# Optimization experiments

Hardware: AMD Instinct MI355X
Metric: run time of the kernel (lower is better)

Reference implementation:

```python
import jax, jax.numpy as jnp
import numpy as np

N_ATOMS = 50000
N_RES = 6250
C_IN = 30
E_DIM = 12
E_BOND = 150000
E_RAD = 800000
E_RES_RAD = 400000
E_CORR = 20000


def _layer_norm(h, g, b, eps=1e-5):
    mu = h.mean(-1, keepdims=True)
    var = ((h - mu) ** 2).mean(-1, keepdims=True)
    return (h - mu) / jnp.sqrt(var + eps) * g + b


def _mlp(h, W, b, g, beta):
    # Seq(Linear, ReLU, LayerNorm, Dropout) in eval mode (dropout = identity)
    return _layer_norm(jax.nn.relu(h @ W + b), g, beta)


def _point_conv(x, pos, src, dst, W, b, g, beta, num_nodes):
    # PyG PointNetConv with add_self_loops=True, aggr='add'
    loops = jnp.arange(num_nodes)
    s = jnp.concatenate([src, loops])
    d = jnp.concatenate([dst, loops])
    msg = jnp.concatenate([x[s], pos[s] - pos[d]], axis=-1)  # [E+N, F+3]
    h = _mlp(msg, W, b, g, beta)
    return jax.ops.segment_sum(h, d, num_segments=num_nodes)


def _gcne_conv(x, edge_index, edge_attr, W, bias):
    # GCNEConv: gcn_norm with self loops, message = cat(x_j, e) @ W * norm + bias, scatter-add
    n = x.shape[0]
    loops = jnp.arange(n)
    s = jnp.concatenate([edge_index[0], loops])
    d = jnp.concatenate([edge_index[1], loops])
    w_full = jnp.ones(s.shape[0], x.dtype)
    deg = jax.ops.segment_sum(w_full, d, num_segments=n)
    dinv = jnp.where(deg > 0, deg ** -0.5, 0.0)
    norm = dinv[s] * dinv[d]
    ea = jnp.concatenate([edge_attr, jnp.zeros((n, edge_attr.shape[1]), edge_attr.dtype)], axis=0)
    msg = (jnp.concatenate([x[s], ea], axis=-1) @ W) * norm[:, None] + bias
    return jax.ops.segment_sum(msg, d, num_segments=n)


def setup_inputs():
    key = jax.random.key(0)
    ks = jax.random.split(key, 20)
    inp = {}
    inp['x'] = jax.random.normal(ks[0], (N_ATOMS, C_IN), jnp.float32)
    inp['pos'] = jax.random.uniform(ks[1], (N_ATOMS, 3), jnp.float32)
    inp['edge_attr'] = jax.random.normal(ks[2], (E_BOND, E_DIM), jnp.float32)
    inp['edge_index'] = jax.random.randint(ks[3], (2, E_BOND), 0, N_ATOMS)
    inp['rad_edge_index'] = jax.random.randint(ks[4], (2, E_RAD), 0, N_ATOMS)
    inp['res_rad_edge_index'] = jax.random.randint(ks[5], (2, E_RES_RAD), 0, N_RES)
    inp['residue_index'] = jnp.sort(jax.random.randint(ks[6], (N_ATOMS,), 0, N_RES))
    inp['src_idx'] = jax.random.randint(ks[7], (E_CORR,), 0, N_RES)
    inp['tgt_idx'] = jax.random.randint(ks[8], (E_CORR,), 0, N_RES)
    inp['y_lab'] = jax.random.randint(ks[9], (E_CORR,), 0, 2).astype(jnp.int32)
    def glorot(k, shape):
        s = (2.0 / (shape[0] + shape[1])) ** 0.5
        return jax.random.normal(k, shape, jnp.float32) * s
    # conv1 local MLP [3+C_IN -> 64]
    inp['w_pc1'] = glorot(ks[10], (C_IN + 3, 64)); inp['b_pc1'] = jnp.zeros(64)
    inp['g_pc1'] = jnp.ones(64); inp['be_pc1'] = jnp.zeros(64)
    # gcn1 weight [C_IN+E_DIM -> 64]
    inp['w_gcn'] = glorot(ks[11], (C_IN + E_DIM, 64)); inp['b_gcn'] = jnp.zeros(64)
    # atom_embed MLP [64 -> 64]
    inp['w_ae'] = glorot(ks[12], (64, 64)); inp['b_ae'] = jnp.zeros(64)
    inp['g_ae'] = jnp.ones(64); inp['be_ae'] = jnp.zeros(64)
    # res_embed MLP [64 -> 64]
    inp['w_re'] = glorot(ks[13], (64, 64)); inp['b_re'] = jnp.zeros(64)
    inp['g_re'] = jnp.ones(64); inp['be_re'] = jnp.zeros(64)
    # res_conv1 local MLP [3+64 -> 128]
    inp['w_rc'] = glorot(ks[14], (64 + 3, 128)); inp['b_rc'] = jnp.zeros(128)
    inp['g_rc'] = jnp.ones(128); inp['be_rc'] = jnp.zeros(128)
    # res_conv1 global MLP [128 -> 128]
    inp['w_rg'] = glorot(ks[15], (128, 128)); inp['b_rg'] = jnp.zeros(128)
    inp['g_rg'] = jnp.ones(128); inp['be_rg'] = jnp.zeros(128)
    return inp


def reference(x, pos, edge_attr,
              w_pc1, b_pc1, g_pc1, be_pc1,
              w_gcn, b_gcn,
              w_ae, b_ae, g_ae, be_ae,
              w_re, b_re, g_re, be_re,
              w_rc, b_rc, g_rc, be_rc,
              w_rg, b_rg, g_rg, be_rg,
              edge_index, rad_edge_index, res_rad_edge_index,
              residue_index, src_idx, tgt_idx, y_lab):
    n = x.shape[0]
    # SAModule 1: PointConv over atom radius graph, aggr='add', no global_nn
    x1 = _point_conv(x, pos, rad_edge_index[0], rad_edge_index[1],
                     w_pc1, b_pc1, g_pc1, be_pc1, n)
    # GCNEConv over bond graph
    x2 = _gcne_conv(x, edge_index, edge_attr, w_gcn, b_gcn)
    atom_x = _mlp(x1 + x2, w_ae, b_ae, g_ae, be_ae)
    # atom -> residue pooling (global_add_pool / global_mean_pool)
    res_x = jax.ops.segment_sum(atom_x, residue_index, num_segments=N_RES)
    cnt = jax.ops.segment_sum(jnp.ones(n, x.dtype), residue_index, num_segments=N_RES)
    res_pos = jax.ops.segment_sum(pos, residue_index, num_segments=N_RES) / jnp.maximum(cnt, 1.0)[:, None]
    res_x = _mlp(res_x, w_re, b_re, g_re, be_re)
    # SAModule 2: PointConv over residue radius graph with global MLP
    x3 = _point_conv(res_x, res_pos, res_rad_edge_index[0], res_rad_edge_index[1],
                     w_rc, b_rc, g_rc, be_rc, N_RES)
    x3 = _mlp(x3, w_rg, b_rg, g_rg, be_rg)
    # correspondence pairs + CosineEmbeddingLoss(reduction='none')
    x_s = x3[src_idx]
    x_t = x3[tgt_idx]
    y = (2 * y_lab - 1).astype(x.dtype)  # {0,1} -> {-1,+1}
    eps = 1e-8
    cos = (x_s * x_t).sum(-1) / (jnp.maximum(jnp.linalg.norm(x_s, axis=-1), eps) *
                                 jnp.maximum(jnp.linalg.norm(x_t, axis=-1), eps))
    unweighted = jnp.where(y == 1, 1.0 - cos, jnp.maximum(cos, 0.0))
    pos_l = jnp.where(y != 1, 0.0, y)
    neg_l = 1.0 - pos_l
    pos_w = neg_l.sum() / pos_l.sum()
    loss = jnp.mean((pos_l * pos_w + neg_l) * unweighted)
    return loss
```

## Files before the change

kernel.cpp:

```cpp
#include <hip/hip_runtime.h>
#include <math.h>

#define N_ATOMS 50000
#define N_RES 6250
#define C_IN 30
#define E_DIM 12
#define E_BOND 150000
#define E_RAD 800000
#define E_RES_RAD 400000
#define E_CORR 20000

__device__ __forceinline__ int rfl(int v) { return __builtin_amdgcn_readfirstlane(v); }

__device__ __forceinline__ float wsum(float v) {
#pragma unroll
  for (int m = 1; m < 64; m <<= 1) v += __shfl_xor(v, m, 64);
  return v;
}

template <int K>
__global__ void rowmat64(const float* __restrict__ X, const float* __restrict__ W,
                         float* __restrict__ out, int nrows) {
  const int lane = threadIdx.x & 63;
  const int wid = (blockIdx.x * blockDim.x + threadIdx.x) >> 6;
  const int nw = (gridDim.x * blockDim.x) >> 6;
  float wcol[K];
#pragma unroll
  for (int k = 0; k < K; k++) wcol[k] = W[k * 64 + lane];
  for (int r = wid; r < nrows; r += nw) {
    float acc = 0.0f;
#pragma unroll
    for (int k = 0; k < K; k++) acc += X[(size_t)r * K + k] * wcol[k];
    out[(size_t)r * 64 + lane] = acc;
  }
}

__global__ void pc1_edge(const float* __restrict__ xw1, const float* __restrict__ pos,
                         const int* __restrict__ src, const int* __restrict__ dst,
                         const float* __restrict__ W, const float* __restrict__ b,
                         const float* __restrict__ g, const float* __restrict__ be,
                         float* __restrict__ acc) {
  const int lane = threadIdx.x & 63;
  const int wid = (blockIdx.x * blockDim.x + threadIdx.x) >> 6;
  const int nw = (gridDim.x * blockDim.x) >> 6;
  const float w0 = W[(C_IN + 0) * 64 + lane];
  const float w1 = W[(C_IN + 1) * 64 + lane];
  const float w2 = W[(C_IN + 2) * 64 + lane];
  const float bb = b[lane], gg = g[lane], eb = be[lane];
  const int total = E_RAD + N_ATOMS;
  for (int e0 = wid * 2; e0 < total; e0 += nw * 2) {
    const int e1 = e0 + 1;
    int sA, dA, sB, dB;
    float dA0 = 0.0f, dA1 = 0.0f, dA2 = 0.0f, dB0 = 0.0f, dB1 = 0.0f, dB2 = 0.0f;
    if (e0 < E_RAD) {
      sA = rfl(src[e0]); dA = rfl(dst[e0]);
      dA0 = pos[sA * 3 + 0] - pos[dA * 3 + 0];
      dA1 = pos[sA * 3 + 1] - pos[dA * 3 + 1];
      dA2 = pos[sA * 3 + 2] - pos[dA * 3 + 2];
    } else {
      sA = dA = e0 - E_RAD;
    }
    if (e1 < E_RAD) {
      sB = rfl(src[e1]); dB = rfl(dst[e1]);
      dB0 = pos[sB * 3 + 0] - pos[dB * 3 + 0];
      dB1 = pos[sB * 3 + 1] - pos[dB * 3 + 1];
      dB2 = pos[sB * 3 + 2] - pos[dB * 3 + 2];
    } else {
      sB = dB = e1 - E_RAD;
    }
    float hA = xw1[(size_t)sA * 64 + lane] + bb + dA0 * w0 + dA1 * w1 + dA2 * w2;
    float hB = xw1[(size_t)sB * 64 + lane] + bb + dB0 * w0 + dB1 * w1 + dB2 * w2;
    hA = fmaxf(hA, 0.0f);
    hB = fmaxf(hB, 0.0f);
    float s1A = hA, s2A = hA * hA, s1B = hB, s2B = hB * hB;
#pragma unroll
    for (int m = 1; m < 64; m <<= 1) {
      s1A += __shfl_xor(s1A, m, 64);
      s2A += __shfl_xor(s2A, m, 64);
      s1B += __shfl_xor(s1B, m, 64);
      s2B += __shfl_xor(s2B, m, 64);
    }
    const float muA = s1A * (1.0f / 64.0f);
    const float muB = s1B * (1.0f / 64.0f);
    const float vaA = s2A * (1.0f / 64.0f) - muA * muA;
    const float vaB = s2B * (1.0f / 64.0f) - muB * muB;
    const float rA = rsqrtf(vaA + 1e-5f);
    const float rB = rsqrtf(vaB + 1e-5f);
    atomicAdd(&acc[(size_t)dA * 64 + lane], (hA - muA) * rA * gg + eb);
    atomicAdd(&acc[(size_t)dB * 64 + lane], (hB - muB) * rB * gg + eb);
  }
}

__global__ void deg_init(float* __restrict__ deg) {
  int i = blockIdx.x * blockDim.x + threadIdx.x;
  if (i < N_ATOMS) deg[i] = 1.0f;
}
__global__ void deg_count(const int* __restrict__ dst, float* __restrict__ deg) {
  int i = blockIdx.x * blockDim.x + threadIdx.x;
  if (i < E_BOND) atomicAdd(&deg[dst[i]], 1.0f);
}
__global__ void deg_inv(float* __restrict__ deg) {
  int i = blockIdx.x * blockDim.x + threadIdx.x;
  if (i < N_ATOMS) deg[i] = rsqrtf(deg[i]);
}

__global__ void gcn_edge(const float* __restrict__ xw2, const float* __restrict__ ea,
                         const int* __restrict__ src, const int* __restrict__ dst,
                         const float* __restrict__ W, const float* __restrict__ b,
                         const float* __restrict__ dinv, float* __restrict__ acc) {
  const int lane = threadIdx.x & 63;
  const int wid = (blockIdx.x * blockDim.x + threadIdx.x) >> 6;
  const int nw = (gridDim.x * blockDim.x) >> 6;
  float we[E_DIM];
#pragma unroll
  for (int k = 0; k < E_DIM; k++) we[k] = W[(C_IN + k) * 64 + lane];
  const float bb = b[lane];
  for (int e = wid; e < E_BOND; e += nw) {
    int s = rfl(src[e]);
    int d = rfl(dst[e]);
    float t = xw2[(size_t)s * 64 + lane];
#pragma unroll
    for (int k = 0; k < E_DIM; k++) t += ea[(size_t)e * E_DIM + k] * we[k];
    t = t * (dinv[s] * dinv[d]) + bb;
    atomicAdd(&acc[(size_t)d * 64 + lane], t);
  }
}

__global__ void atom_embed(const float* __restrict__ acc12, const float* __restrict__ xw2,
                           const float* __restrict__ dinv, const float* __restrict__ bgcn,
                           const float* __restrict__ pos, const int* __restrict__ resid,
                           const float* __restrict__ W, const float* __restrict__ b,
                           const float* __restrict__ g, const float* __restrict__ be,
                           float* __restrict__ res_acc, float* __restrict__ res_pacc,
                           float* __restrict__ res_cnt) {
  const int lane = threadIdx.x & 63;
  const int wid = (blockIdx.x * blockDim.x + threadIdx.x) >> 6;
  const int nw = (gridDim.x * blockDim.x) >> 6;
  const float bb = b[lane], gg = g[lane], eb = be[lane], bg = bgcn[lane];
  for (int r = wid; r < N_ATOMS; r += nw) {
    const float di = dinv[r];
    float vin = acc12[(size_t)r * 64 + lane] + xw2[(size_t)r * 64 + lane] * di * di + bg;
    float acc = bb;
#pragma unroll 8
    for (int k = 0; k < 64; k++) {
      float xv = __shfl(vin, k, 64);
      acc += xv * W[k * 64 + lane];
    }
    float h = fmaxf(acc, 0.0f);
    float s1 = h, s2 = h * h;
#pragma unroll
    for (int m = 1; m < 64; m <<= 1) {
      s1 += __shfl_xor(s1, m, 64);
      s2 += __shfl_xor(s2, m, 64);
    }
    float mu = s1 * (1.0f / 64.0f);
    float var = s2 * (1.0f / 64.0f) - mu * mu;
    float v = (h - mu) * rsqrtf(var + 1e-5f) * gg + eb;
    int rr = resid[r];
    atomicAdd(&res_acc[(size_t)rr * 64 + lane], v);
    if (lane < 3) atomicAdd(&res_pacc[rr * 3 + lane], pos[r * 3 + lane]);
    if (lane == 3) atomicAdd(&res_cnt[rr], 1.0f);
  }
}

__global__ void res_embed(const float* __restrict__ racc, const float* __restrict__ pacc,
                          const float* __restrict__ cnt, const float* __restrict__ W,
                          const float* __restrict__ b, const float* __restrict__ g,
                          const float* __restrict__ be, float* __restrict__ res_x,
                          float* __restrict__ res_pos) {
  const int lane = threadIdx.x & 63;
  const int wid = (blockIdx.x * blockDim.x + threadIdx.x) >> 6;
  const int nw = (gridDim.x * blockDim.x) >> 6;
  const float bb = b[lane], gg = g[lane], eb = be[lane];
  for (int r = wid; r < N_RES; r += nw) {
    float vin = racc[(size_t)r * 64 + lane];
    float acc = bb;
#pragma unroll 8
    for (int k = 0; k < 64; k++) {
      float xv = __shfl(vin, k, 64);
      acc += xv * W[k * 64 + lane];
    }
    float h = fmaxf(acc, 0.0f);
    float s1 = h, s2 = h * h;
#pragma unroll
    for (int m = 1; m < 64; m <<= 1) {
      s1 += __shfl_xor(s1, m, 64);
      s2 += __shfl_xor(s2, m, 64);
    }
    float mu = s1 * (1.0f / 64.0f);
    float var = s2 * (1.0f / 64.0f) - mu * mu;
    res_x[(size_t)r * 64 + lane] = (h - mu) * rsqrtf(var + 1e-5f) * gg + eb;
    if (lane < 3) res_pos[r * 3 + lane] = pacc[r * 3 + lane] / fmaxf(cnt[r], 1.0f);
  }
}

__global__ void rc_pre(const float* __restrict__ rx, const float* __restrict__ W,
                       const float* __restrict__ b, float* __restrict__ rw) {
  const int lane = threadIdx.x & 63;
  const int wid = (blockIdx.x * blockDim.x + threadIdx.x) >> 6;
  const int nw = (gridDim.x * blockDim.x) >> 6;
  for (int r = wid; r < N_RES; r += nw) {
    float vin = rx[(size_t)r * 64 + lane];
    float a0 = b[lane], a1 = b[64 + lane];
#pragma unroll 8
    for (int k = 0; k < 64; k++) {
      float xv = __shfl(vin, k, 64);
      a0 += xv * W[k * 128 + lane];
      a1 += xv * W[k * 128 + 64 + lane];
    }
    rw[(size_t)r * 128 + lane] = a0;
    rw[(size_t)r * 128 + 64 + lane] = a1;
  }
}

__global__ void rc_edge(const float* __restrict__ rw, const float* __restrict__ rpos,
                        const int* __restrict__ src, const int* __restrict__ dst,
                        const float* __restrict__ W, const float* __restrict__ g,
                        const float* __restrict__ be, float* __restrict__ acc) {
  const int lane = threadIdx.x & 63;
  const int wid = (blockIdx.x * blockDim.x + threadIdx.x) >> 6;
  const int nw = (gridDim.x * blockDim.x) >> 6;
  float wa[3], wb[3];
#pragma unroll
  for (int i = 0; i < 3; i++) {
    wa[i] = W[(64 + i) * 128 + lane];
    wb[i] = W[(64 + i) * 128 + 64 + lane];
  }
  const float g0 = g[lane], g1 = g[64 + lane], e0c = be[lane], e1c = be[64 + lane];
  const int total = E_RES_RAD + N_RES;
  for (int e0 = wid * 2; e0 < total; e0 += nw * 2) {
    const int e1 = e0 + 1;
    int sA, dA, sB, dB;
    float dA0 = 0.0f, dA1 = 0.0f, dA2 = 0.0f, dB0 = 0.0f, dB1 = 0.0f, dB2 = 0.0f;
    if (e0 < E_RES_RAD) {
      sA = rfl(src[e0]); dA = rfl(dst[e0]);
      dA0 = rpos[sA * 3 + 0] - rpos[dA * 3 + 0];
      dA1 = rpos[sA * 3 + 1] - rpos[dA * 3 + 1];
      dA2 = rpos[sA * 3 + 2] - rpos[dA * 3 + 2];
    } else {
      sA = dA = e0 - E_RES_RAD;
    }
    if (e1 < E_RES_RAD) {
      sB = rfl(src[e1]); dB = rfl(dst[e1]);
      dB0 = rpos[sB * 3 + 0] - rpos[dB * 3 + 0];
      dB1 = rpos[sB * 3 + 1] - rpos[dB * 3 + 1];
      dB2 = rpos[sB * 3 + 2] - rpos[dB * 3 + 2];
    } else {
      sB = dB = e1 - E_RES_RAD;
    }
    float hA0 = rw[(size_t)sA * 128 + lane]      + dA0 * wa[0] + dA1 * wa[1] + dA2 * wa[2];
    float hA1 = rw[(size_t)sA * 128 + 64 + lane] + dA0 * wb[0] + dA1 * wb[1] + dA2 * wb[2];
    float hB0 = rw[(size_t)sB * 128 + lane]      + dB0 * wa[0] + dB1 * wa[1] + dB2 * wa[2];
    float hB1 = rw[(size_t)sB * 128 + 64 + lane] + dB0 * wb[0] + dB1 * wb[1] + dB2 * wb[2];
    hA0 = fmaxf(hA0, 0.0f); hA1 = fmaxf(hA1, 0.0f);
    hB0 = fmaxf(hB0, 0.0f); hB1 = fmaxf(hB1, 0.0f);
    float s1A = hA0 + hA1, s2A = hA0 * hA0 + hA1 * hA1;
    float s1B = hB0 + hB1, s2B = hB0 * hB0 + hB1 * hB1;
#pragma unroll
    for (int m = 1; m < 64; m <<= 1) {
      s1A += __shfl_xor(s1A, m, 64);
      s2A += __shfl_xor(s2A, m, 64);
      s1B += __shfl_xor(s1B, m, 64);
      s2B += __shfl_xor(s2B, m, 64);
    }
    const float muA = s1A * (1.0f / 128.0f);
    const float muB = s1B * (1.0f / 128.0f);
    const float vaA = s2A * (1.0f / 128.0f) - muA * muA;
    const float vaB = s2B * (1.0f / 128.0f) - muB * muB;
    const float rsA = rsqrtf(vaA + 1e-5f);
    const float rsB = rsqrtf(vaB + 1e-5f);
    atomicAdd(&acc[(size_t)dA * 128 + lane],      (hA0 - muA) * rsA * g0 + e0c);
    atomicAdd(&acc[(size_t)dA * 128 + 64 + lane], (hA1 - muA) * rsA * g1 + e1c);
    atomicAdd(&acc[(size_t)dB * 128 + lane],      (hB0 - muB) * rsB * g0 + e0c);
    atomicAdd(&acc[(size_t)dB * 128 + 64 + lane], (hB1 - muB) * rsB * g1 + e1c);
  }
}

__global__ void rg_embed(const float* __restrict__ acc, const float* __restrict__ W,
                         const float* __restrict__ b, const float* __restrict__ g,
                         const float* __restrict__ be, float* __restrict__ x3) {
  const int lane = threadIdx.x & 63;
  const int wid = (blockIdx.x * blockDim.x + threadIdx.x) >> 6;
  const int nw = (gridDim.x * blockDim.x) >> 6;
  for (int r = wid; r < N_RES; r += nw) {
    float i0 = acc[(size_t)r * 128 + lane];
    float i1 = acc[(size_t)r * 128 + 64 + lane];
    float a0 = b[lane], a1 = b[64 + lane];
#pragma unroll 8
    for (int k = 0; k < 64; k++) {
      float x0 = __shfl(i0, k, 64);
      float x1 = __shfl(i1, k, 64);
      a0 += x0 * W[k * 128 + lane] + x1 * W[(k + 64) * 128 + lane];
      a1 += x0 * W[k * 128 + 64 + lane] + x1 * W[(k + 64) * 128 + 64 + lane];
    }
    float h0 = fmaxf(a0, 0.0f), h1 = fmaxf(a1, 0.0f);
    float s1 = h0 + h1, s2 = h0 * h0 + h1 * h1;
#pragma unroll
    for (int m = 1; m < 64; m <<= 1) {
      s1 += __shfl_xor(s1, m, 64);
      s2 += __shfl_xor(s2, m, 64);
    }
    float mu = s1 * (1.0f / 128.0f);
    float var = s2 * (1.0f / 128.0f) - mu * mu;
    float rs = rsqrtf(var + 1e-5f);
    x3[(size_t)r * 128 + lane] = (h0 - mu) * rs * g[lane] + be[lane];
    x3[(size_t)r * 128 + 64 + lane] = (h1 - mu) * rs * g[64 + lane] + be[64 + lane];
  }
}

__global__ void loss_pairs(const float* __restrict__ x3, const int* __restrict__ si,
                           const int* __restrict__ ti, const int* __restrict__ y,
                           float* __restrict__ lacc) {
  const int lane = threadIdx.x & 63;
  const int wid = (blockIdx.x * blockDim.x + threadIdx.x) >> 6;
  const int nw = (gridDim.x * blockDim.x) >> 6;
  float sp = 0.0f, sn = 0.0f, cp = 0.0f, cn = 0.0f;
  for (int p = wid; p < E_CORR; p += nw) {
    int a = rfl(si[p]), bI = rfl(ti[p]), yy = rfl(y[p]);
    float a0 = x3[(size_t)a * 128 + lane], a1 = x3[(size_t)a * 128 + 64 + lane];
    float b0 = x3[(size_t)bI * 128 + lane], b1 = x3[(size_t)bI * 128 + 64 + lane];
    float dot = a0 * b0 + a1 * b1;
    float na = a0 * a0 + a1 * a1;
    float nb = b0 * b0 + b1 * b1;
#pragma unroll
    for (int m = 1; m < 64; m <<= 1) {
      dot += __shfl_xor(dot, m, 64);
      na += __shfl_xor(na, m, 64);
      nb += __shfl_xor(nb, m, 64);
    }
    float cosv = dot / (fmaxf(sqrtf(na), 1e-8f) * fmaxf(sqrtf(nb), 1e-8f));
    if (yy == 1) {
      sp += 1.0f - cosv;
      cp += 1.0f;
    } else {
      sn += fmaxf(cosv, 0.0f);
      cn += 1.0f;
    }
  }
  if (lane == 0) {
    atomicAdd(&lacc[0], sp);
    atomicAdd(&lacc[1], sn);
    atomicAdd(&lacc[2], cp);
    atomicAdd(&lacc[3], cn);
  }
}

__global__ void finalize(const float* __restrict__ lacc, float* __restrict__ out) {
  if (blockIdx.x == 0 && threadIdx.x == 0) {
    float pw = lacc[3] / lacc[2];
    out[0] = (lacc[0] * pw + lacc[1]) / (float)E_CORR;
  }
}

extern "C" void kernel_launch(void* const* d_in, const int* in_sizes, int n_in,
                              void* d_out, int out_size, void* d_ws, size_t ws_size,
                              hipStream_t stream) {
  const float* x = (const float*)d_in[0];
  const float* pos = (const float*)d_in[1];
  const float* edge_attr = (const float*)d_in[2];
  const int* edge_index = (const int*)d_in[3];
  const int* rad_ei = (const int*)d_in[4];
  const int* res_rad_ei = (const int*)d_in[5];
  const int* resid = (const int*)d_in[6];
  const int* src_idx = (const int*)d_in[7];
  const int* tgt_idx = (const int*)d_in[8];
  const int* y_lab = (const int*)d_in[9];
  const float* w_pc1 = (const float*)d_in[10];
  const float* b_pc1 = (const float*)d_in[11];
  const float* g_pc1 = (const float*)d_in[12];
  const float* be_pc1 = (const float*)d_in[13];
  const float* w_gcn = (const float*)d_in[14];
  const float* b_gcn = (const float*)d_in[15];
  const float* w_ae = (const float*)d_in[16];
  const float* b_ae = (const float*)d_in[17];
  const float* g_ae = (const float*)d_in[18];
  const float* be_ae = (const float*)d_in[19];
  const float* w_re = (const float*)d_in[20];
  const float* b_re = (const float*)d_in[21];
  const float* g_re = (const float*)d_in[22];
  const float* be_re = (const float*)d_in[23];
  const float* w_rc = (const float*)d_in[24];
  const float* b_rc = (const float*)d_in[25];
  const float* g_rc = (const float*)d_in[26];
  const float* be_rc = (const float*)d_in[27];
  const float* w_rg = (const float*)d_in[28];
  const float* b_rg = (const float*)d_in[29];
  const float* g_rg = (const float*)d_in[30];
  const float* be_rg = (const float*)d_in[31];

  float* ws = (float*)d_ws;
  float* acc12 = ws;
  float* res_acc = acc12 + (size_t)N_ATOMS * 64;
  float* res_pacc = res_acc + (size_t)N_RES * 64;
  float* res_cnt = res_pacc + 18752;
  float* x3acc = res_cnt + 6272;
  float* lacc = x3acc + (size_t)N_RES * 128;
  size_t zero_floats = (size_t)N_ATOMS * 64 + (size_t)N_RES * 64 + 18752 + 6272 +
                       (size_t)N_RES * 128 + 8;
  float* xw1 = lacc + 8;
  float* xw2 = xw1 + (size_t)N_ATOMS * 64;
  float* deg = xw2 + (size_t)N_ATOMS * 64;
  float* res_x = deg + N_ATOMS;
  float* res_pos = res_x + (size_t)N_RES * 64;
  float* rw = res_pos + 18752;
  float* x3 = rw + (size_t)N_RES * 128;

  hipMemsetAsync(d_ws, 0, zero_floats * sizeof(float), stream);

  const int B = 256;
  const int GB = 2048;
  const int GS = 512;

  rowmat64<C_IN><<<GB, B, 0, stream>>>(x, w_pc1, xw1, N_ATOMS);
  pc1_edge<<<GB, B, 0, stream>>>(xw1, pos, rad_ei, rad_ei + E_RAD, w_pc1, b_pc1, g_pc1,
                                 be_pc1, acc12);

  deg_init<<<(N_ATOMS + B - 1) / B, B, 0, stream>>>(deg);
  deg_count<<<(E_BOND + B - 1) / B, B, 0, stream>>>(edge_index + E_BOND, deg);
  deg_inv<<<(N_ATOMS + B - 1) / B, B, 0, stream>>>(deg);

  rowmat64<C_IN><<<GB, B, 0, stream>>>(x, w_gcn, xw2, N_ATOMS);
  gcn_edge<<<GB, B, 0, stream>>>(xw2, edge_attr, edge_index, edge_index + E_BOND, w_gcn,
                                 b_gcn, deg, acc12);

  atom_embed<<<GB, B, 0, stream>>>(acc12, xw2, deg, b_gcn, pos, resid, w_ae, b_ae, g_ae,
                                   be_ae, res_acc, res_pacc, res_cnt);

  res_embed<<<GS, B, 0, stream>>>(res_acc, res_pacc, res_cnt, w_re, b_re, g_re, be_re,
                                  res_x, res_pos);

  rc_pre<<<GS, B, 0, stream>>>(res_x, w_rc, b_rc, rw);
  rc_edge<<<GB, B, 0, stream>>>(rw, res_pos, res_rad_ei, res_rad_ei + E_RES_RAD, w_rc,
                                g_rc, be_rc, x3acc);
  rg_embed<<<GS, B, 0, stream>>>(x3acc, w_rg, b_rg, g_rg, be_rg, x3);

  loss_pairs<<<GS, B, 0, stream>>>(x3, src_idx, tgt_idx, y_lab, lacc);
  finalize<<<1, 64, 0, stream>>>(lacc, (float*)d_out);
}
```

Baseline: 772.9 us.

## Replace atomic scatter in point convs with CSR dst-sorted gather

```diff
diff --git a/kernel.cpp b/kernel.cpp
--- a/kernel.cpp
+++ b/kernel.cpp
@@ -12,12 +12,6 @@
 
 __device__ __forceinline__ int rfl(int v) { return __builtin_amdgcn_readfirstlane(v); }
 
-__device__ __forceinline__ float wsum(float v) {
-#pragma unroll
-  for (int m = 1; m < 64; m <<= 1) v += __shfl_xor(v, m, 64);
-  return v;
-}
-
 template <int K>
 __global__ void rowmat64(const float* __restrict__ X, const float* __restrict__ W,
                          float* __restrict__ out, int nrows) {
@@ -35,43 +29,93 @@
   }
 }
 
-__global__ void pc1_edge(const float* __restrict__ xw1, const float* __restrict__ pos,
-                         const int* __restrict__ src, const int* __restrict__ dst,
-                         const float* __restrict__ W, const float* __restrict__ b,
-                         const float* __restrict__ g, const float* __restrict__ be,
-                         float* __restrict__ acc) {
-  const int lane = threadIdx.x & 63;
-  const int wid = (blockIdx.x * blockDim.x + threadIdx.x) >> 6;
-  const int nw = (gridDim.x * blockDim.x) >> 6;
+__global__ void hist_kernel(const int* __restrict__ dst, int* __restrict__ cnt, int n) {
+  int i = blockIdx.x * blockDim.x + threadIdx.x;
+  if (i < n) atomicAdd(&cnt[dst[i]], 1);
+}
+
+__global__ void ex_scan(const int* __restrict__ cnt, int* __restrict__ cur, int n) {
+  __shared__ int wsums[16];
+  __shared__ int carry_s;
+  const int tid = threadIdx.x;
+  const int lane = tid & 63;
+  const int w = tid >> 6;
+  if (tid == 0) carry_s = 0;
+  __syncthreads();
+  for (int base = 0; base < n; base += 1024) {
+    int i = base + tid;
+    int v = (i < n) ? cnt[i] : 0;
+    int s = v;
+#pragma unroll
+    for (int m = 1; m < 64; m <<= 1) {
+      int t = __shfl_up(s, m, 64);
+      if (lane >= m) s += t;
+    }
+    if (lane == 63) wsums[w] = s;
+    __syncthreads();
+    if (w == 0) {
+      int x = (lane < 16) ? wsums[lane] : 0;
+#pragma unroll
+      for (int m = 1; m < 16; m <<= 1) {
+        int t = __shfl_up(x, m, 64);
+        if (lane >= m) x += t;
+      }
+      if (lane < 16) wsums[lane] = x;
+    }
+    __syncthreads();
+    const int woff = (w > 0) ? wsums[w - 1] : 0;
+    const int carry = carry_s;
+    if (i < n) cur[i] = carry + woff + (s - v);
+    __syncthreads();
+    if (tid == 1023) carry_s = carry + wsums[15];
+    __syncthreads();
+  }
+}
+
+__global__ void scat_kernel(const int* __restrict__ src, const int* __restrict__ dst,
+                            int* __restrict__ cur, int* __restrict__ ss, int n) {
+  int e = blockIdx.x * blockDim.x + threadIdx.x;
+  if (e < n) {
+    int p = atomicAdd(&cur[dst[e]], 1);
+    ss[p] = src[e];
+  }
+}
+
+__global__ void pc1_gather(const float* __restrict__ xw1, const float* __restrict__ pos,
+                           const int* __restrict__ ss, const int* __restrict__ cur,
+                           const float* __restrict__ W, const float* __restrict__ b,
+                           const float* __restrict__ g, const float* __restrict__ be,
+                           float* __restrict__ acc) {
+  const int lane = threadIdx.x & 63;
+  const int d = (blockIdx.x * blockDim.x + threadIdx.x) >> 6;
+  if (d >= N_ATOMS) return;
   const float w0 = W[(C_IN + 0) * 64 + lane];
   const float w1 = W[(C_IN + 1) * 64 + lane];
   const float w2 = W[(C_IN + 2) * 64 + lane];
   const float bb = b[lane], gg = g[lane], eb = be[lane];
-  const int total = E_RAD + N_ATOMS;
-  for (int e0 = wid * 2; e0 < total; e0 += nw * 2) {
-    const int e1 = e0 + 1;
-    int sA, dA, sB, dB;
-    float dA0 = 0.0f, dA1 = 0.0f, dA2 = 0.0f, dB0 = 0.0f, dB1 = 0.0f, dB2 = 0.0f;
-    if (e0 < E_RAD) {
-      sA = rfl(src[e0]); dA = rfl(dst[e0]);
-      dA0 = pos[sA * 3 + 0] - pos[dA * 3 + 0];
-      dA1 = pos[sA * 3 + 1] - pos[dA * 3 + 1];
-      dA2 = pos[sA * 3 + 2] - pos[dA * 3 + 2];
-    } else {
-      sA = dA = e0 - E_RAD;
-    }
-    if (e1 < E_RAD) {
-      sB = rfl(src[e1]); dB = rfl(dst[e1]);
-      dB0 = pos[sB * 3 + 0] - pos[dB * 3 + 0];
-      dB1 = pos[sB * 3 + 1] - pos[dB * 3 + 1];
-      dB2 = pos[sB * 3 + 2] - pos[dB * 3 + 2];
-    } else {
-      sB = dB = e1 - E_RAD;
-    }
-    float hA = xw1[(size_t)sA * 64 + lane] + bb + dA0 * w0 + dA1 * w1 + dA2 * w2;
-    float hB = xw1[(size_t)sB * 64 + lane] + bb + dB0 * w0 + dB1 * w1 + dB2 * w2;
-    hA = fmaxf(hA, 0.0f);
-    hB = fmaxf(hB, 0.0f);
+  const int beg = rfl(d ? cur[d - 1] : 0);
+  const int end = rfl(cur[d]);
+  const float pd0 = pos[d * 3 + 0], pd1 = pos[d * 3 + 1], pd2 = pos[d * 3 + 2];
+  float h = fmaxf(xw1[(size_t)d * 64 + lane] + bb, 0.0f);
+  float s1 = h, s2 = h * h;
+#pragma unroll
+  for (int m = 1; m < 64; m <<= 1) {
+    s1 += __shfl_xor(s1, m, 64);
+    s2 += __shfl_xor(s2, m, 64);
+  }
+  float mu = s1 * (1.0f / 64.0f);
+  float var = s2 * (1.0f / 64.0f) - mu * mu;
+  float accv = (h - mu) * rsqrtf(var + 1e-5f) * gg + eb;
+  int j = beg;
+  for (; j + 1 < end; j += 2) {
+    const int sA = rfl(ss[j]);
+    const int sB = rfl(ss[j + 1]);
+    const float dA0 = pos[sA * 3 + 0] - pd0, dA1 = pos[sA * 3 + 1] - pd1,
+                dA2 = pos[sA * 3 + 2] - pd2;
+    const float dB0 = pos[sB * 3 + 0] - pd0, dB1 = pos[sB * 3 + 1] - pd1,
+                dB2 = pos[sB * 3 + 2] - pd2;
+    float hA = fmaxf(xw1[(size_t)sA * 64 + lane] + bb + dA0 * w0 + dA1 * w1 + dA2 * w2, 0.0f);
+    float hB = fmaxf(xw1[(size_t)sB * 64 + lane] + bb + dB0 * w0 + dB1 * w1 + dB2 * w2, 0.0f);
     float s1A = hA, s2A = hA * hA, s1B = hB, s2B = hB * hB;
 #pragma unroll
     for (int m = 1; m < 64; m <<= 1) {
@@ -80,15 +124,28 @@
       s1B += __shfl_xor(s1B, m, 64);
       s2B += __shfl_xor(s2B, m, 64);
     }
-    const float muA = s1A * (1.0f / 64.0f);
-    const float muB = s1B * (1.0f / 64.0f);
+    const float muA = s1A * (1.0f / 64.0f), muB = s1B * (1.0f / 64.0f);
     const float vaA = s2A * (1.0f / 64.0f) - muA * muA;
     const float vaB = s2B * (1.0f / 64.0f) - muB * muB;
-    const float rA = rsqrtf(vaA + 1e-5f);
-    const float rB = rsqrtf(vaB + 1e-5f);
-    atomicAdd(&acc[(size_t)dA * 64 + lane], (hA - muA) * rA * gg + eb);
-    atomicAdd(&acc[(size_t)dB * 64 + lane], (hB - muB) * rB * gg + eb);
-  }
+    accv += (hA - muA) * rsqrtf(vaA + 1e-5f) * gg + eb;
+    accv += (hB - muB) * rsqrtf(vaB + 1e-5f) * gg + eb;
+  }
+  if (j < end) {
+    const int sA = rfl(ss[j]);
+    const float dA0 = pos[sA * 3 + 0] - pd0, dA1 = pos[sA * 3 + 1] - pd1,
+                dA2 = pos[sA * 3 + 2] - pd2;
+    float hA = fmaxf(xw1[(size_t)sA * 64 + lane] + bb + dA0 * w0 + dA1 * w1 + dA2 * w2, 0.0f);
+    float s1A = hA, s2A = hA * hA;
+#pragma unroll
+    for (int m = 1; m < 64; m <<= 1) {
+      s1A += __shfl_xor(s1A, m, 64);
+      s2A += __shfl_xor(s2A, m, 64);
+    }
+    const float muA = s1A * (1.0f / 64.0f);
+    const float vaA = s2A * (1.0f / 64.0f) - muA * muA;
+    accv += (hA - muA) * rsqrtf(vaA + 1e-5f) * gg + eb;
+  }
+  acc[(size_t)d * 64 + lane] = accv;
 }
 
 __global__ void deg_init(float* __restrict__ deg) {
@@ -213,13 +270,13 @@
   }
 }
 
-__global__ void rc_edge(const float* __restrict__ rw, const float* __restrict__ rpos,
-                        const int* __restrict__ src, const int* __restrict__ dst,
-                        const float* __restrict__ W, const float* __restrict__ g,
-                        const float* __restrict__ be, float* __restrict__ acc) {
-  const int lane = threadIdx.x & 63;
-  const int wid = (blockIdx.x * blockDim.x + threadIdx.x) >> 6;
-  const int nw = (gridDim.x * blockDim.x) >> 6;
+__global__ void rc_gather(const float* __restrict__ rw, const float* __restrict__ rpos,
+                          const int* __restrict__ ss, const int* __restrict__ cur,
+                          const float* __restrict__ W, const float* __restrict__ g,
+                          const float* __restrict__ be, float* __restrict__ out) {
+  const int lane = threadIdx.x & 63;
+  const int d = (blockIdx.x * blockDim.x + threadIdx.x) >> 6;
+  if (d >= N_RES) return;
   float wa[3], wb[3];
 #pragma unroll
   for (int i = 0; i < 3; i++) {
@@ -227,33 +284,34 @@
     wb[i] = W[(64 + i) * 128 + 64 + lane];
   }
   const float g0 = g[lane], g1 = g[64 + lane], e0c = be[lane], e1c = be[64 + lane];
-  const int total = E_RES_RAD + N_RES;
-  for (int e0 = wid * 2; e0 < total; e0 += nw * 2) {
-    const int e1 = e0 + 1;
-    int sA, dA, sB, dB;
-    float dA0 = 0.0f, dA1 = 0.0f, dA2 = 0.0f, dB0 = 0.0f, dB1 = 0.0f, dB2 = 0.0f;
-    if (e0 < E_RES_RAD) {
-      sA = rfl(src[e0]); dA = rfl(dst[e0]);
-      dA0 = rpos[sA * 3 + 0] - rpos[dA * 3 + 0];
-      dA1 = rpos[sA * 3 + 1] - rpos[dA * 3 + 1];
-      dA2 = rpos[sA * 3 + 2] - rpos[dA * 3 + 2];
-    } else {
-      sA = dA = e0 - E_RES_RAD;
-    }
-    if (e1 < E_RES_RAD) {
-      sB = rfl(src[e1]); dB = rfl(dst[e1]);
-      dB0 = rpos[sB * 3 + 0] - rpos[dB * 3 + 0];
-      dB1 = rpos[sB * 3 + 1] - rpos[dB * 3 + 1];
-      dB2 = rpos[sB * 3 + 2] - rpos[dB * 3 + 2];
-    } else {
-      sB = dB = e1 - E_RES_RAD;
-    }
-    float hA0 = rw[(size_t)sA * 128 + lane]      + dA0 * wa[0] + dA1 * wa[1] + dA2 * wa[2];
-    float hA1 = rw[(size_t)sA * 128 + 64 + lane] + dA0 * wb[0] + dA1 * wb[1] + dA2 * wb[2];
-    float hB0 = rw[(size_t)sB * 128 + lane]      + dB0 * wa[0] + dB1 * wa[1] + dB2 * wa[2];
-    float hB1 = rw[(size_t)sB * 128 + 64 + lane] + dB0 * wb[0] + dB1 * wb[1] + dB2 * wb[2];
-    hA0 = fmaxf(hA0, 0.0f); hA1 = fmaxf(hA1, 0.0f);
-    hB0 = fmaxf(hB0, 0.0f); hB1 = fmaxf(hB1, 0.0f);
+  const int beg = rfl(d ? cur[d - 1] : 0);
+  const int end = rfl(cur[d]);
+  const float pd0 = rpos[d * 3 + 0], pd1 = rpos[d * 3 + 1], pd2 = rpos[d * 3 + 2];
+  float h0 = fmaxf(rw[(size_t)d * 128 + lane], 0.0f);
+  float h1 = fmaxf(rw[(size_t)d * 128 + 64 + lane], 0.0f);
+  float s1 = h0 + h1, s2 = h0 * h0 + h1 * h1;
+#pragma unroll
+  for (int m = 1; m < 64; m <<= 1) {
+    s1 += __shfl_xor(s1, m, 64);
+    s2 += __shfl_xor(s2, m, 64);
+  }
+  float mu = s1 * (1.0f / 128.0f);
+  float var = s2 * (1.0f / 128.0f) - mu * mu;
+  float rs = rsqrtf(var + 1e-5f);
+  float a0 = (h0 - mu) * rs * g0 + e0c;
+  float a1 = (h1 - mu) * rs * g1 + e1c;
+  int j = beg;
+  for (; j + 1 < end; j += 2) {
+    const int sA = rfl(ss[j]);
+    const int sB = rfl(ss[j + 1]);
+    const float dA0 = rpos[sA * 3 + 0] - pd0, dA1 = rpos[sA * 3 + 1] - pd1,
+                dA2 = rpos[sA * 3 + 2] - pd2;
+    const float dB0 = rpos[sB * 3 + 0] - pd0, dB1 = rpos[sB * 3 + 1] - pd1,
+                dB2 = rpos[sB * 3 + 2] - pd2;
+    float hA0 = fmaxf(rw[(size_t)sA * 128 + lane]      + dA0 * wa[0] + dA1 * wa[1] + dA2 * wa[2], 0.0f);
+    float hA1 = fmaxf(rw[(size_t)sA * 128 + 64 + lane] + dA0 * wb[0] + dA1 * wb[1] + dA2 * wb[2], 0.0f);
+    float hB0 = fmaxf(rw[(size_t)sB * 128 + lane]      + dB0 * wa[0] + dB1 * wa[1] + dB2 * wa[2], 0.0f);
+    float hB1 = fmaxf(rw[(size_t)sB * 128 + 64 + lane] + dB0 * wb[0] + dB1 * wb[1] + dB2 * wb[2], 0.0f);
     float s1A = hA0 + hA1, s2A = hA0 * hA0 + hA1 * hA1;
     float s1B = hB0 + hB1, s2B = hB0 * hB0 + hB1 * hB1;
 #pragma unroll
@@ -263,17 +321,33 @@
       s1B += __shfl_xor(s1B, m, 64);
       s2B += __shfl_xor(s2B, m, 64);
     }
-    const float muA = s1A * (1.0f / 128.0f);
-    const float muB = s1B * (1.0f / 128.0f);
+    const float muA = s1A * (1.0f / 128.0f), muB = s1B * (1.0f / 128.0f);
     const float vaA = s2A * (1.0f / 128.0f) - muA * muA;
     const float vaB = s2B * (1.0f / 128.0f) - muB * muB;
+    const float rsA = rsqrtf(vaA + 1e-5f), rsB = rsqrtf(vaB + 1e-5f);
+    a0 += (hA0 - muA) * rsA * g0 + e0c + (hB0 - muB) * rsB * g0 + e0c;
+    a1 += (hA1 - muA) * rsA * g1 + e1c + (hB1 - muB) * rsB * g1 + e1c;
+  }
+  if (j < end) {
+    const int sA = rfl(ss[j]);
+    const float dA0 = rpos[sA * 3 + 0] - pd0, dA1 = rpos[sA * 3 + 1] - pd1,
+                dA2 = rpos[sA * 3 + 2] - pd2;
+    float hA0 = fmaxf(rw[(size_t)sA * 128 + lane]      + dA0 * wa[0] + dA1 * wa[1] + dA2 * wa[2], 0.0f);
+    float hA1 = fmaxf(rw[(size_t)sA * 128 + 64 + lane] + dA0 * wb[0] + dA1 * wb[1] + dA2 * wb[2], 0.0f);
+    float s1A = hA0 + hA1, s2A = hA0 * hA0 + hA1 * hA1;
+#pragma unroll
+    for (int m = 1; m < 64; m <<= 1) {
+      s1A += __shfl_xor(s1A, m, 64);
+      s2A += __shfl_xor(s2A, m, 64);
+    }
+    const float muA = s1A * (1.0f / 128.0f);
+    const float vaA = s2A * (1.0f / 128.0f) - muA * muA;
     const float rsA = rsqrtf(vaA + 1e-5f);
-    const float rsB = rsqrtf(vaB + 1e-5f);
-    atomicAdd(&acc[(size_t)dA * 128 + lane],      (hA0 - muA) * rsA * g0 + e0c);
-    atomicAdd(&acc[(size_t)dA * 128 + 64 + lane], (hA1 - muA) * rsA * g1 + e1c);
-    atomicAdd(&acc[(size_t)dB * 128 + lane],      (hB0 - muB) * rsB * g0 + e0c);
-    atomicAdd(&acc[(size_t)dB * 128 + 64 + lane], (hB1 - muB) * rsB * g1 + e1c);
-  }
+    a0 += (hA0 - muA) * rsA * g0 + e0c;
+    a1 += (hA1 - muA) * rsA * g1 + e1c;
+  }
+  out[(size_t)d * 128 + lane] = a0;
+  out[(size_t)d * 128 + 64 + lane] = a1;
 }
 
 __global__ void rg_embed(const float* __restrict__ acc, const float* __restrict__ W,
@@ -389,37 +463,48 @@
   const float* be_rg = (const float*)d_in[31];
 
   float* ws = (float*)d_ws;
-  float* acc12 = ws;
-  float* res_acc = acc12 + (size_t)N_ATOMS * 64;
-  float* res_pacc = res_acc + (size_t)N_RES * 64;
+  float* res_acc = ws;
+  float* res_pacc = res_acc + 400000;
   float* res_cnt = res_pacc + 18752;
-  float* x3acc = res_cnt + 6272;
-  float* lacc = x3acc + (size_t)N_RES * 128;
-  size_t zero_floats = (size_t)N_ATOMS * 64 + (size_t)N_RES * 64 + 18752 + 6272 +
-                       (size_t)N_RES * 128 + 8;
-  float* xw1 = lacc + 8;
-  float* xw2 = xw1 + (size_t)N_ATOMS * 64;
-  float* deg = xw2 + (size_t)N_ATOMS * 64;
-  float* res_x = deg + N_ATOMS;
-  float* res_pos = res_x + (size_t)N_RES * 64;
+  float* lacc = res_cnt + 6272;
+  int* cnt_pc1 = (int*)(lacc + 8);
+  int* cnt_rc = cnt_pc1 + 50048;
+  size_t zero_elems = 400000 + 18752 + 6272 + 8 + 50048 + 6272;
+  int* cur_pc1 = cnt_rc + 6272;
+  int* cur_rc = cur_pc1 + 50048;
+  int* ss_pc1 = cur_rc + 6272;
+  int* ss_rc = ss_pc1 + 800000;
+  float* xw1 = (float*)(ss_rc + 400000);
+  float* xw2 = xw1 + 3200000;
+  float* deg = xw2 + 3200000;
+  float* acc12 = deg + 50000;
+  float* res_x = acc12 + 3200000;
+  float* res_pos = res_x + 400000;
   float* rw = res_pos + 18752;
-  float* x3 = rw + (size_t)N_RES * 128;
-
-  hipMemsetAsync(d_ws, 0, zero_floats * sizeof(float), stream);
+  float* x3m = acc12;
+  float* x3 = rw;
+
+  hipMemsetAsync(d_ws, 0, zero_elems * sizeof(float), stream);
 
   const int B = 256;
   const int GB = 2048;
   const int GS = 512;
 
   rowmat64<C_IN><<<GB, B, 0, stream>>>(x, w_pc1, xw1, N_ATOMS);
-  pc1_edge<<<GB, B, 0, stream>>>(xw1, pos, rad_ei, rad_ei + E_RAD, w_pc1, b_pc1, g_pc1,
-                                 be_pc1, acc12);
+  rowmat64<C_IN><<<GB, B, 0, stream>>>(x, w_gcn, xw2, N_ATOMS);
+
+  hist_kernel<<<(E_RAD + B - 1) / B, B, 0, stream>>>(rad_ei + E_RAD, cnt_pc1, E_RAD);
+  ex_scan<<<1, 1024, 0, stream>>>(cnt_pc1, cur_pc1, N_ATOMS);
+  scat_kernel<<<(E_RAD + B - 1) / B, B, 0, stream>>>(rad_ei, rad_ei + E_RAD, cur_pc1,
+                                                     ss_pc1, E_RAD);
+  pc1_gather<<<(N_ATOMS * 64 + B - 1) / B, B, 0, stream>>>(xw1, pos, ss_pc1, cur_pc1,
+                                                           w_pc1, b_pc1, g_pc1, be_pc1,
+                                                           acc12);
 
   deg_init<<<(N_ATOMS + B - 1) / B, B, 0, stream>>>(deg);
   deg_count<<<(E_BOND + B - 1) / B, B, 0, stream>>>(edge_index + E_BOND, deg);
   deg_inv<<<(N_ATOMS + B - 1) / B, B, 0, stream>>>(deg);
 
-  rowmat64<C_IN><<<GB, B, 0, stream>>>(x, w_gcn, xw2, N_ATOMS);
   gcn_edge<<<GB, B, 0, stream>>>(xw2, edge_attr, edge_index, edge_index + E_BOND, w_gcn,
                                  b_gcn, deg, acc12);
 
@@ -429,10 +514,17 @@
   res_embed<<<GS, B, 0, stream>>>(res_acc, res_pacc, res_cnt, w_re, b_re, g_re, be_re,
                                   res_x, res_pos);
 
+  hist_kernel<<<(E_RES_RAD + B - 1) / B, B, 0, stream>>>(res_rad_ei + E_RES_RAD, cnt_rc,
+                                                         E_RES_RAD);
+  ex_scan<<<1, 1024, 0, stream>>>(cnt_rc, cur_rc, N_RES);
+  scat_kernel<<<(E_RES_RAD + B - 1) / B, B, 0, stream>>>(res_rad_ei,
+                                                         res_rad_ei + E_RES_RAD, cur_rc,
+                                                         ss_rc, E_RES_RAD);
+
   rc_pre<<<GS, B, 0, stream>>>(res_x, w_rc, b_rc, rw);
-  rc_edge<<<GB, B, 0, stream>>>(rw, res_pos, res_rad_ei, res_rad_ei + E_RES_RAD, w_rc,
-                                g_rc, be_rc, x3acc);
-  rg_embed<<<GS, B, 0, stream>>>(x3acc, w_rg, b_rg, g_rg, be_rg, x3);
+  rc_gather<<<(N_RES * 64 + B - 1) / B, B, 0, stream>>>(rw, res_pos, ss_rc, cur_rc, w_rc,
+                                                        g_rc, be_rc, x3m);
+  rg_embed<<<GS, B, 0, stream>>>(x3m, w_rg, b_rg, g_rg, be_rg, x3);
 
   loss_pairs<<<GS, B, 0, stream>>>(x3, src_idx, tgt_idx, y_lab, lacc);
   finalize<<<1, 64, 0, stream>>>(lacc, (float*)d_out);
```

Result: slower. 790.7 us (+2.3%).
